# Kernel tuning notes

Hardware: AMD Instinct MI355X
Metric: run time of the kernel (lower is better)

## Reference

```python
import jax, jax.numpy as jnp
import numpy as np

D_MODEL = 256
NUM_HEADS = 4
D_HEAD = D_MODEL // NUM_HEADS
LN_EPS = 1e-5
NEG_INF = -1e9


def setup_inputs() -> dict:
    key = jax.random.key(0)
    ks = jax.random.split(key, 8)
    B, N = 4, 2048
    s = 1.0 / np.sqrt(D_MODEL)
    return {
        "x": jax.random.normal(ks[0], (B, N, D_MODEL), dtype=jnp.float32),
        "Wq": jax.random.normal(ks[1], (D_MODEL, D_MODEL), dtype=jnp.float32) * s,
        "Wk": jax.random.normal(ks[2], (D_MODEL, D_MODEL), dtype=jnp.float32) * s,
        "Wv": jax.random.normal(ks[3], (D_MODEL, D_MODEL), dtype=jnp.float32) * s,
        "Wo": jax.random.normal(ks[4], (D_MODEL, D_MODEL), dtype=jnp.float32) * s,
        "bo": jnp.zeros((D_MODEL,), dtype=jnp.float32),
        "gamma": jnp.ones((D_MODEL,), dtype=jnp.float32),
        "beta": jnp.zeros((D_MODEL,), dtype=jnp.float32),
        "k_neighbors": 8,
    }


def build_knn_adj(x, k):
    # x: [B, N, D]; returns symmetric 0/1 adjacency [B, N, N]
    B, N, _ = x.shape
    xn = x / jnp.maximum(jnp.linalg.norm(x, axis=-1, keepdims=True), 1e-12)
    sim = jnp.einsum('bnd,bmd->bnm', xn, xn)  # [B, N, N]
    _, idx = jax.lax.top_k(sim, k + 1)        # [B, N, k+1]
    b = jnp.arange(B)[:, None, None]
    r = jnp.arange(N)[None, :, None]
    adj = jnp.zeros((B, N, N), dtype=jnp.float32).at[b, r, idx].add(1.0)
    adj = jnp.maximum(adj, jnp.swapaxes(adj, 1, 2))
    return adj


def layer_norm(x, gamma, beta):
    mu = jnp.mean(x, axis=-1, keepdims=True)
    var = jnp.mean(jnp.square(x - mu), axis=-1, keepdims=True)
    return (x - mu) * jax.lax.rsqrt(var + LN_EPS) * gamma + beta


def reference(x, Wq, Wk, Wv, Wo, bo, gamma, beta, k_neighbors):
    B, N, D = x.shape
    adj = build_knn_adj(x, k_neighbors)  # [B, N, N]

    def split_heads(t):  # [B, N, D] -> [B, H, N, d]
        return jnp.transpose(t.reshape(B, N, NUM_HEADS, D_HEAD), (0, 2, 1, 3))

    q = split_heads(x @ Wq)
    k = split_heads(x @ Wk)
    v = split_heads(x @ Wv)

    scores = jnp.einsum('bhnd,bhmd->bhnm', q, k) / jnp.sqrt(jnp.float32(D_HEAD))
    scores = jnp.where(adj[:, None, :, :] > 0, scores, NEG_INF)
    attn = jax.nn.softmax(scores, axis=-1)  # dropout is identity at inference
    out = jnp.einsum('bhnm,bhmd->bhnd', attn, v)
    out = jnp.transpose(out, (0, 2, 1, 3)).reshape(B, N, D)
    out = out @ Wo + bo
    return layer_norm(x + out, gamma, beta)
```

## Files before the change

### kernel.cpp

```cpp
#include <hip/hip_runtime.h>
#include <hip/hip_bf16.h>
#include <math.h>

#define BATCH 4
#define N 2048
#define D 256
#define NH 4
#define DH 64
#define TOPK 9
#define NEG_BIG -1e30f

typedef __bf16 bf16;
typedef __bf16 bf16x4 __attribute__((ext_vector_type(4)));
typedef __bf16 bf16x8 __attribute__((ext_vector_type(8)));
typedef float f32x4 __attribute__((ext_vector_type(4)));

#define PK3(a,b,c) ((a) | ((b) << 2) | ((c) << 4))
#define PK6(a,b,c,d,e,f) ((a) | ((b) << 2) | ((c) << 4) | ((d) << 6) | ((e) << 8) | ((f) << 10))

#define WAITVM(Nc) __builtin_amdgcn_s_waitcnt((((Nc) & 0xf)) | (7u << 4) | (0xfu << 8) | ((((unsigned)(Nc)) >> 4) << 14))

__device__ __forceinline__ void async_cp16(const bf16* g, const bf16* l) {
  __builtin_amdgcn_global_load_lds(
      (const __attribute__((address_space(1))) void*)(uintptr_t)g,
      (__attribute__((address_space(3))) void*)(uintptr_t)l, 16, 0, 0);
}

__global__ __launch_bounds__(64) void prep_kernel(const float* __restrict__ x,
                                                  const float* __restrict__ Wq,
                                                  const float* __restrict__ Wk,
                                                  const float* __restrict__ Wv,
                                                  const float* __restrict__ Wo,
                                                  bf16* __restrict__ XsN,
                                                  bf16* __restrict__ Wt,
                                                  float* __restrict__ norms,
                                                  uint4* __restrict__ mask4) {
  int blk = blockIdx.x;
  int lane = threadIdx.x;
  if (blk < 8192) {
    float4 v = *(const float4*)(x + (size_t)blk * D + lane * 4);
    float ss = v.x * v.x + v.y * v.y + v.z * v.z + v.w * v.w;
    for (int off = 32; off; off >>= 1) ss += __shfl_down(ss, off);
    ss = __shfl(ss, 0);
    float nrm = fmaxf(sqrtf(ss), 1e-12f);
    if (lane == 0) norms[blk] = nrm;
    float sc = 1.0f / nrm;
    float xs[4] = {v.x * sc, v.y * sc, v.z * sc, v.w * sc};
    bf16* o = XsN + (size_t)blk * 512 + lane * 4;
#pragma unroll
    for (int j = 0; j < 4; ++j) {
      float xv = xs[j];
      bf16 h = (bf16)xv;
      o[j] = h;
      o[256 + j] = (bf16)(xv - (float)h);
    }
  } else if (blk < 9216) {
    int jj = blk - 8192;
    const float* W = (jj < 256) ? Wq : (jj < 512) ? Wk : (jj < 768) ? Wv : Wo;
    int j = jj & 255;
    bf16* dst = Wt + (size_t)jj * 512;
    for (int k = lane; k < 256; k += 64) {
      float w = W[(size_t)k * D + j];
      bf16 h = (bf16)w;
      dst[k] = h;
      dst[256 + k] = (bf16)(w - (float)h);
    }
  } else {
    int base = (blk - 9216) * 1024 + lane;
#pragma unroll
    for (int t = 0; t < 16; ++t)
      mask4[base + t * 64] = make_uint4(0, 0, 0, 0);
  }
}

__device__ __forceinline__ void gemm_core(bf16* As, bf16* Bs,
                                          const bf16* __restrict__ Ab,
                                          const bf16* __restrict__ Bb,
                                          void* __restrict__ Cvoid,
                                          int lda, int ldb, int ldc,
                                          int nsteps, int amap, int bmap,
                                          int row0, int col0,
                                          int outmode, bool mirror,
                                          const float* __restrict__ rowscale) {
  int tid = threadIdx.x;
  int lane = tid & 63;
  int wv = tid >> 6;
  int wm = (wv >> 1) * 64;
  int wn = (wv & 1) * 64;

  int rbase = tid >> 2;
  int gperm = (tid & 3) ^ ((rbase >> 1) & 3);
  const bf16* ga0 = Ab + (size_t)rbase * lda + gperm * 8;
  const bf16* gb0 = Bb + (size_t)rbase * ldb + gperm * 8;
  int ldsoff = tid * 8;

  int fr = lane & 15;
  int G = lane >> 4;

  f32x4 acc[4][4] = {};

  auto issue = [&](int st, int buf) {
    int ch = st >> 3;
    int aoff = (((amap >> (ch * 2)) & 3) << 8) | ((st & 7) << 5);
    int boff = (((bmap >> (ch * 2)) & 3) << 8) | ((st & 7) << 5);
#pragma unroll
    for (int q = 0; q < 2; ++q)
      async_cp16(ga0 + (size_t)q * 64 * lda + aoff, &As[buf * 4096 + ldsoff + q * 2048]);
#pragma unroll
    for (int q = 0; q < 2; ++q)
      async_cp16(gb0 + (size_t)q * 64 * ldb + boff, &Bs[buf * 4096 + ldsoff + q * 2048]);
  };

  issue(0, 0);
  for (int st = 0; st < nsteps; ++st) {
    int buf = st & 1;
    if (st + 1 < nsteps) {
      issue(st + 1, buf ^ 1);
      WAITVM(4);
    } else {
      WAITVM(0);
    }
    __builtin_amdgcn_s_barrier();
    bf16x8 af[4], bfr[4];
#pragma unroll
    for (int mi = 0; mi < 4; ++mi) {
      int r = wm + mi * 16 + fr;
      af[mi] = *(const bf16x8*)&As[buf * 4096 + r * 32 + ((G ^ ((r >> 1) & 3)) << 3)];
    }
#pragma unroll
    for (int nj = 0; nj < 4; ++nj) {
      int r = wn + nj * 16 + fr;
      bfr[nj] = *(const bf16x8*)&Bs[buf * 4096 + r * 32 + ((G ^ ((r >> 1) & 3)) << 3)];
    }
#pragma unroll
    for (int mi = 0; mi < 4; ++mi)
#pragma unroll
      for (int nj = 0; nj < 4; ++nj)
        acc[mi][nj] = __builtin_amdgcn_mfma_f32_16x16x32_bf16(af[mi], bfr[nj], acc[mi][nj], 0, 0, 0);
    __builtin_amdgcn_s_barrier();
  }

  int er = (lane >> 4) * 4;
  int ec = lane & 15;
#pragma unroll
  for (int mi = 0; mi < 4; ++mi) {
    int rb = row0 + wm + mi * 16 + er;
    float scl[4] = {1.f, 1.f, 1.f, 1.f};
    if (rowscale) {
      float4 s4 = *(const float4*)(rowscale + rb);
      scl[0] = s4.x; scl[1] = s4.y; scl[2] = s4.z; scl[3] = s4.w;
    }
#pragma unroll
    for (int nj = 0; nj < 4; ++nj) {
      int cb = col0 + wn + nj * 16 + ec;
      if (outmode == 1) {
        float* Cb = (float*)Cvoid;
#pragma unroll
        for (int reg = 0; reg < 4; ++reg)
          __builtin_nontemporal_store(acc[mi][nj][reg],
                                      &Cb[(size_t)(rb + reg) * ldc + cb]);
        if (mirror) {
#pragma unroll
          for (int reg = 0; reg < 4; ++reg)
            __builtin_nontemporal_store(acc[mi][nj][reg],
                                        &Cb[(size_t)cb * ldc + rb + reg]);
        }
      } else {
        bf16* Cb = (bf16*)Cvoid;
#pragma unroll
        for (int reg = 0; reg < 4; ++reg)
          Cb[(size_t)(rb + reg) * ldc + cb] = (bf16)(acc[mi][nj][reg] * scl[reg]);
      }
    }
  }
}

__global__ __launch_bounds__(256, 4) void gemm_sim_kernel(const bf16* __restrict__ XsN,
                                                          float* __restrict__ sim,
                                                          int amap, int bmap) {
  __shared__ bf16 As[2 * 128 * 32];
  __shared__ bf16 Bs[2 * 128 * 32];
  int g = blockIdx.x;
  int xcd = g & 7;
  int slot = g >> 3;
  int z = xcd >> 1;
  int t = (xcd & 1) * 68 + slot;
  int by = 0;
  while (t >= 16 - by) { t -= 16 - by; ++by; }
  int bx = by + t;
  gemm_core(As, Bs,
            XsN + (size_t)z * N * 512 + (size_t)by * 128 * 512,
            XsN + (size_t)z * N * 512 + (size_t)bx * 128 * 512,
            sim + (size_t)z * N * N,
            512, 512, N, 24, amap, bmap, by * 128, bx * 128,
            1, bx != by, nullptr);
}

__global__ __launch_bounds__(256, 4) void gemm_qkv_kernel(const bf16* __restrict__ XsN,
                                                          const bf16* __restrict__ Wt,
                                                          bf16* __restrict__ qkv,
                                                          int amap, int bmap,
                                                          const float* __restrict__ norms) {
  __shared__ bf16 As[2 * 128 * 32];
  __shared__ bf16 Bs[2 * 128 * 32];
  gemm_core(As, Bs,
            XsN + (size_t)blockIdx.y * 128 * 512,
            Wt + (size_t)blockIdx.x * 128 * 512,
            qkv, 512, 512, 768, 16, amap, bmap,
            blockIdx.y * 128, blockIdx.x * 128, 2, false, norms);
}

__global__ __launch_bounds__(256, 4) void gemm_fused_kernel(const bf16* __restrict__ XsN,
                                                            float* __restrict__ sim,
                                                            int amap_s, int bmap_s,
                                                            const bf16* __restrict__ Wt,
                                                            bf16* __restrict__ qkv,
                                                            int amap_q, int bmap_q,
                                                            const float* __restrict__ norms) {
  __shared__ bf16 As[2 * 128 * 32];
  __shared__ bf16 Bs[2 * 128 * 32];
  int g = blockIdx.x;
  if (g < 544) {
    int xcd = g & 7;
    int slot = g >> 3;
    int z = xcd >> 1;
    int t = (xcd & 1) * 68 + slot;
    int by = 0;
    while (t >= 16 - by) { t -= 16 - by; ++by; }
    int bx = by + t;
    gemm_core(As, Bs,
              XsN + (size_t)z * N * 512 + (size_t)by * 128 * 512,
              XsN + (size_t)z * N * 512 + (size_t)bx * 128 * 512,
              sim + (size_t)z * N * N,
              512, 512, N, 24, amap_s, bmap_s, by * 128, bx * 128,
              1, bx != by, nullptr);
  } else {
    int t = g - 544;
    int xcd = t & 7;
    int slot = t >> 3;
    int by = (xcd >> 1) * 16 + (xcd & 1) * 8 + slot / 6;
    int bx = slot % 6;
    gemm_core(As, Bs,
              XsN + (size_t)by * 128 * 512,
              Wt + (size_t)bx * 128 * 512,
              qkv, 512, 512, 768, 16, amap_q, bmap_q,
              by * 128, bx * 128, 2, false, norms);
  }
}

__global__ __launch_bounds__(64) void topk_adj_kernel(const float* __restrict__ sim,
                                                      unsigned* __restrict__ mask) {
  int row = blockIdx.x;
  int lane = threadIdx.x;
  int b = row >> 11, r = row & 2047;
  const float* srow = sim + (size_t)row * N;
  float v[32];
#pragma unroll
  for (int it = 0; it < 8; ++it) {
    float4 q = *(const float4*)(srow + it * 256 + lane * 4);
    v[it * 4 + 0] = q.x; v[it * 4 + 1] = q.y;
    v[it * 4 + 2] = q.z; v[it * 4 + 3] = q.w;
  }
  unsigned removed = 0;
  for (int rs = 0; rs < TOPK; ++rs) {
    float m = -3e38f;
    int mi = 0;
#pragma unroll
    for (int i = 0; i < 32; ++i) {
      float vv = ((removed >> i) & 1u) ? -3e38f : v[i];
      if (vv > m) { m = vv; mi = i; }
    }
    int gidx = ((mi >> 2) << 8) + lane * 4 + (mi & 3);
    for (int off = 32; off; off >>= 1) {
      float om = __shfl_down(m, off);
      int og = __shfl_down(gidx, off);
      if (om > m || (om == m && og < gidx)) { m = om; gidx = og; }
    }
    gidx = __shfl(gidx, 0);
    if (((gidx >> 2) & 63) == lane)
      removed |= 1u << (((gidx >> 8) << 2) | (gidx & 3));
    if (lane == 0) {
      atomicOr(&mask[(size_t)row * 64 + (gidx >> 5)], 1u << (gidx & 31));
      atomicOr(&mask[(((size_t)b << 11) + gidx) * 64 + (r >> 5)], 1u << (r & 31));
    }
  }
}

__global__ __launch_bounds__(256) void attn_kernel(const bf16* __restrict__ qkv,
                                                   const unsigned* __restrict__ mask,
                                                   bf16* __restrict__ aos) {
  __shared__ float sq[4][256];
  __shared__ unsigned short nbr[4][2048];
  __shared__ int s_nn[4];
  int wv = threadIdx.x >> 6;
  int lane = threadIdx.x & 63;
  int g = blockIdx.x;
  int xcd = g & 7;
  int b = xcd >> 1;
  int tile = (xcd & 1) * 256 + (g >> 3);
  int bn = b * N + tile * 4 + wv;
  if (lane == 0) s_nn[wv] = 0;
  {
    bf16x4 qv = *(const bf16x4*)(qkv + (size_t)bn * 768 + lane * 4);
#pragma unroll
    for (int j = 0; j < 4; ++j) sq[wv][lane * 4 + j] = (float)qv[j];
  }
  __syncthreads();
  unsigned bits = mask[(size_t)bn * (N / 32) + lane];
  while (bits) {
    int bit = __ffs(bits) - 1;
    bits &= bits - 1;
    int p = atomicAdd(&s_nn[wv], 1);
    nbr[wv][p] = (unsigned short)(lane * 32 + bit);
  }
  __syncthreads();
  int nn = s_nn[wv];
  const bf16* base = qkv + (size_t)b * N * 768;
  float acc[4] = {0.f, 0.f, 0.f, 0.f};

  auto score4 = [&](int j, float* s) {
    const bf16* kr = base + (size_t)j * 768 + 256;
#pragma unroll
    for (int h = 0; h < 4; ++h) {
      float a = 0.f;
#pragma unroll
      for (int c = 0; c < DH; c += 8) {
        bf16x8 kk = *(const bf16x8*)(kr + h * DH + c);
#pragma unroll
        for (int t = 0; t < 8; ++t) a += sq[wv][h * DH + c + t] * (float)kk[t];
      }
      s[h] = a * 0.125f;
    }
  };

  if (nn <= 64) {
    float s[4] = {NEG_BIG, NEG_BIG, NEG_BIG, NEG_BIG};
    if (lane < nn) score4(nbr[wv][lane], s);
    float w[4], l[4];
#pragma unroll
    for (int h = 0; h < 4; ++h) {
      float m = s[h];
      for (int off = 32; off; off >>= 1) m = fmaxf(m, __shfl_down(m, off));
      m = __shfl(m, 0);
      float e = (lane < nn) ? __expf(s[h] - m) : 0.f;
      float ls = e;
      for (int off = 32; off; off >>= 1) ls += __shfl_down(ls, off);
      l[h] = __shfl(ls, 0);
      w[h] = e;
    }
    int i = 0;
    for (; i + 4 <= nn; i += 4) {
      int j0 = nbr[wv][i + 0], j1 = nbr[wv][i + 1];
      int j2 = nbr[wv][i + 2], j3 = nbr[wv][i + 3];
      const bf16* p0 = base + (size_t)j0 * 768 + 512;
      const bf16* p1 = base + (size_t)j1 * 768 + 512;
      const bf16* p2 = base + (size_t)j2 * 768 + 512;
      const bf16* p3 = base + (size_t)j3 * 768 + 512;
#pragma unroll
      for (int h = 0; h < 4; ++h) {
        acc[h] += __shfl(w[h], i + 0) * (float)p0[h * DH + lane] +
                  __shfl(w[h], i + 1) * (float)p1[h * DH + lane] +
                  __shfl(w[h], i + 2) * (float)p2[h * DH + lane] +
                  __shfl(w[h], i + 3) * (float)p3[h * DH + lane];
      }
    }
    for (; i < nn; ++i) {
      const bf16* p0 = base + (size_t)nbr[wv][i] * 768 + 512;
#pragma unroll
      for (int h = 0; h < 4; ++h) acc[h] += __shfl(w[h], i) * (float)p0[h * DH + lane];
    }
#pragma unroll
    for (int h = 0; h < 4; ++h) acc[h] /= l[h];
  } else {
    float m[4] = {NEG_BIG, NEG_BIG, NEG_BIG, NEG_BIG};
    for (int i0 = 0; i0 < nn; i0 += 64) {
      float s[4] = {NEG_BIG, NEG_BIG, NEG_BIG, NEG_BIG};
      if (i0 + lane < nn) score4(nbr[wv][i0 + lane], s);
#pragma unroll
      for (int h = 0; h < 4; ++h) m[h] = fmaxf(m[h], s[h]);
    }
#pragma unroll
    for (int h = 0; h < 4; ++h) {
      for (int off = 32; off; off >>= 1) m[h] = fmaxf(m[h], __shfl_down(m[h], off));
      m[h] = __shfl(m[h], 0);
    }
    float l[4] = {0.f, 0.f, 0.f, 0.f};
    for (int i0 = 0; i0 < nn; i0 += 64) {
      float s[4] = {NEG_BIG, NEG_BIG, NEG_BIG, NEG_BIG};
      if (i0 + lane < nn) score4(nbr[wv][i0 + lane], s);
      float e[4];
#pragma unroll
      for (int h = 0; h < 4; ++h) {
        e[h] = (i0 + lane < nn) ? __expf(s[h] - m[h]) : 0.f;
        float ls = e[h];
        for (int off = 32; off; off >>= 1) ls += __shfl_down(ls, off);
        l[h] += __shfl(ls, 0);
      }
      int lim = min(64, nn - i0);
      for (int ii = 0; ii < lim; ++ii) {
        const bf16* p0 = base + (size_t)nbr[wv][i0 + ii] * 768 + 512;
#pragma unroll
        for (int h = 0; h < 4; ++h) acc[h] += __shfl(e[h], ii) * (float)p0[h * DH + lane];
      }
    }
#pragma unroll
    for (int h = 0; h < 4; ++h) acc[h] /= l[h];
  }
#pragma unroll
  for (int h = 0; h < 4; ++h) {
    float a = acc[h];
    bf16 hi = (bf16)a;
    aos[(size_t)bn * 512 + h * DH + lane] = hi;
    aos[(size_t)bn * 512 + 256 + h * DH + lane] = (bf16)(a - (float)hi);
  }
}

__global__ __launch_bounds__(256) void projln_kernel(const bf16* __restrict__ A,
                                                     const bf16* __restrict__ Bw,
                                                     const float* __restrict__ x,
                                                     const float* __restrict__ bo,
                                                     const float* __restrict__ gamma,
                                                     const float* __restrict__ beta,
                                                     float* __restrict__ out) {
  __shared__ bf16 As[2 * 32 * 32];
  __shared__ bf16 Bs[2 * 256 * 32];
  __shared__ float rsum[32][4];
  __shared__ float rsq[32][4];
  int tid = threadIdx.x;
  int lane = tid & 63;
  int wv = tid >> 6;
  int wn = wv * 64;
  int row0 = blockIdx.x * 32;

  int rt = tid >> 2;
  int ra = tid >> 2;
  int gpa = (tid & 3) ^ ((ra >> 1) & 3);
  const bf16* ga0 = A + (size_t)(row0 + ra) * 512 + gpa * 8;

  int fr = lane & 15;
  int G = lane >> 4;

  f32x4 acc[2][4] = {};

  auto issue = [&](int st, int buf) {
    int aoff = ((st >> 3) << 8) | ((st & 7) << 5);
    int boff = (st & 7) << 5;
    if (tid < 128)
      async_cp16(ga0 + aoff, &As[buf * 1024 + tid * 8]);
#pragma unroll
    for (int q = 0; q < 4; ++q) {
      int rb = q * 64 + rt;
      int gpb = (tid & 3) ^ ((rb >> 1) & 3);
      async_cp16(Bw + (size_t)rb * 512 + gpb * 8 + boff,
                 &Bs[buf * 8192 + (q * 256 + tid) * 8]);
    }
  };

  issue(0, 0);
  for (int st = 0; st < 16; ++st) {
    int buf = st & 1;
    if (st + 1 < 16) {
      issue(st + 1, buf ^ 1);
      WAITVM(4);
    } else {
      WAITVM(0);
    }
    __builtin_amdgcn_s_barrier();
    bf16x8 af[2], bfr[4];
#pragma unroll
    for (int mi = 0; mi < 2; ++mi) {
      int r = mi * 16 + fr;
      af[mi] = *(const bf16x8*)&As[buf * 1024 + r * 32 + ((G ^ ((r >> 1) & 3)) << 3)];
    }
#pragma unroll
    for (int nj = 0; nj < 4; ++nj) {
      int r = wn + nj * 16 + fr;
      bfr[nj] = *(const bf16x8*)&Bs[buf * 8192 + r * 32 + ((G ^ ((r >> 1) & 3)) << 3)];
    }
#pragma unroll
    for (int mi = 0; mi < 2; ++mi)
#pragma unroll
      for (int nj = 0; nj < 4; ++nj)
        acc[mi][nj] = __builtin_amdgcn_mfma_f32_16x16x32_bf16(af[mi], bfr[nj], acc[mi][nj], 0, 0, 0);
    __builtin_amdgcn_s_barrier();
  }

  int er = (lane >> 4) * 4;
  int ec = lane & 15;
  float bo_c[4], ga_c[4], be_c[4];
#pragma unroll
  for (int nj = 0; nj < 4; ++nj) {
    int c = wn + nj * 16 + ec;
    bo_c[nj] = bo[c]; ga_c[nj] = gamma[c]; be_c[nj] = beta[c];
  }
#pragma unroll
  for (int mi = 0; mi < 2; ++mi)
#pragma unroll
    for (int reg = 0; reg < 4; ++reg) {
      int rloc = mi * 16 + er + reg;
      const float* xr = x + (size_t)(row0 + rloc) * D;
      float su = 0.f, s2 = 0.f;
#pragma unroll
      for (int nj = 0; nj < 4; ++nj) {
        float u = acc[mi][nj][reg] + bo_c[nj] + xr[wn + nj * 16 + ec];
        su += u; s2 += u * u;
      }
#pragma unroll
      for (int m = 1; m <= 8; m <<= 1) {
        su += __shfl_xor(su, m);
        s2 += __shfl_xor(s2, m);
      }
      if (ec == 0) { rsum[rloc][wv] = su; rsq[rloc][wv] = s2; }
    }
  __syncthreads();
#pragma unroll
  for (int mi = 0; mi < 2; ++mi)
#pragma unroll
    for (int reg = 0; reg < 4; ++reg) {
      int rloc = mi * 16 + er + reg;
      float s = rsum[rloc][0] + rsum[rloc][1] + rsum[rloc][2] + rsum[rloc][3];
      float q2 = rsq[rloc][0] + rsq[rloc][1] + rsq[rloc][2] + rsq[rloc][3];
      float mean = s * (1.0f / D);
      float var = q2 * (1.0f / D) - mean * mean;
      float rstd = rsqrtf(var + 1e-5f);
      const float* xr = x + (size_t)(row0 + rloc) * D;
      float* orow = out + (size_t)(row0 + rloc) * D;
#pragma unroll
      for (int nj = 0; nj < 4; ++nj) {
        float u = acc[mi][nj][reg] + bo_c[nj] + xr[wn + nj * 16 + ec];
        orow[wn + nj * 16 + ec] = (u - mean) * rstd * ga_c[nj] + be_c[nj];
      }
    }
}

extern "C" void kernel_launch(void* const* d_in, const int* in_sizes, int n_in,
                              void* d_out, int out_size, void* d_ws, size_t ws_size,
                              hipStream_t stream) {
  const float* x     = (const float*)d_in[0];
  const float* Wq    = (const float*)d_in[1];
  const float* Wk    = (const float*)d_in[2];
  const float* Wv    = (const float*)d_in[3];
  const float* Wo    = (const float*)d_in[4];
  const float* bo    = (const float*)d_in[5];
  const float* gamma = (const float*)d_in[6];
  const float* beta  = (const float*)d_in[7];
  float* out = (float*)d_out;

  char* ws = (char*)d_ws;
  bf16* XsN      = (bf16*)(ws);
  float* sim     = (float*)(ws + 12582912);
  float* norms   = (float*)(ws + 79691776);
  unsigned* mask = (unsigned*)(ws + 79986688);
  bf16* Wt       = (bf16*)(ws + 82083840);

  bool big = ws_size >= (size_t)125000000;
  bf16* qkv = (bf16*)(ws + (big ? 83132416 : 12582912));
  bf16* aos = (bf16*)(ws + (big ? 95715328 : 37748736));

  const int AMAP_SIM = PK6(0, 0, 1, 0, 0, 0);
  const int BMAP_SIM = PK6(0, 1, 0, 0, 0, 0);
  const int AMAP_2T  = PK3(0, 1, 0);
  const int BMAP_2T  = PK3(0, 0, 1);

  prep_kernel<<<9344, 64, 0, stream>>>(x, Wq, Wk, Wv, Wo, XsN, Wt, norms,
                                       (uint4*)mask);

  if (big) {
    gemm_fused_kernel<<<928, 256, 0, stream>>>(
        XsN, sim, AMAP_SIM, BMAP_SIM, Wt, qkv, AMAP_2T, BMAP_2T, norms);
    topk_adj_kernel<<<BATCH * N, 64, 0, stream>>>(sim, mask);
  } else {
    gemm_sim_kernel<<<544, 256, 0, stream>>>(XsN, sim, AMAP_SIM, BMAP_SIM);
    topk_adj_kernel<<<BATCH * N, 64, 0, stream>>>(sim, mask);
    gemm_qkv_kernel<<<dim3(6, 64), 256, 0, stream>>>(XsN, Wt, qkv,
                                                     AMAP_2T, BMAP_2T, norms);
  }

  attn_kernel<<<(BATCH * N) / 4, 256, 0, stream>>>(qkv, mask, aos);

  projln_kernel<<<256, 256, 0, stream>>>(aos, Wt + (size_t)768 * 512,
                                         x, bo, gamma, beta, out);
}
```

Baseline: 186.4 us.

## Replace 128x128 fused GEMM with 256x256-tile, 8-wave MFMA kernel

Replaces the fused similarity/QKV GEMM, which used 128x128 tiles with 4 waves, by a 256x256-tile kernel with 8 waves. It uses a 64-wide K slab in 128KB of LDS, split-phase staging of A and B with async global-to-LDS copies, and s_setprio around the MFMA bursts. Grid scheduling is remapped to 144 symmetric sim tiles plus 96 QKV tiles, with XCD-aware placement. The goal is higher arithmetic intensity and less global/LDS traffic per FLOP. The cost is fewer blocks (240), so occupancy and load balance across CUs drop.

New measurement: 189.8 us. Within noise of the previous version (+1.9%).

```diff
diff --git a/kernel.cpp b/kernel.cpp
--- a/kernel.cpp
+++ b/kernel.cpp
@@ -73,6 +73,190 @@
   }
 }
 
+__device__ __forceinline__ void gemm_core256(bf16* S,
+                                             const bf16* __restrict__ Ab,
+                                             const bf16* __restrict__ Bb,
+                                             void* __restrict__ Cvoid,
+                                             int ldc, int ntiles,
+                                             int amap, int bmap,
+                                             int row0, int col0,
+                                             int outmode, bool mirror,
+                                             const float* __restrict__ rowscale) {
+  int tid = threadIdx.x;
+  int lane = tid & 63;
+  int wv = tid >> 6;
+  int wm = (wv >> 2) * 128;
+  int wn = (wv & 3) * 64;
+  int aht = wv >> 2;
+  int bht = 2 + ((wv & 3) >> 1);
+  int brow = (wv & 1) * 64;
+
+  int fr = lane & 15;
+  int fq = lane >> 4;
+
+  int s0 = tid, s1 = tid + 512;
+  int r0 = s0 >> 3, sl0 = s0 & 7;
+  int r1 = s1 >> 3, sl1 = s1 & 7;
+  int gc0 = (sl0 ^ (r0 & 7)) << 3;
+  int gc1 = (sl1 ^ (r1 & 7)) << 3;
+
+  f32x4 acc[8][4] = {};
+
+  auto koffs = [&](int kt, int map) {
+    return (((map >> ((kt >> 2) * 2)) & 3) << 8) | ((kt & 3) << 6);
+  };
+  auto stageAB = [&](int kt, int buf, int half01) {
+    const bf16* Base = half01 ? Bb : Ab;
+    int koff = koffs(kt, half01 ? bmap : amap);
+    bf16* d = S + buf * 32768 + half01 * 16384;
+    const bf16* b0 = Base + koff;
+    async_cp16(b0 + (size_t)r0 * 512 + gc0, d + s0 * 8);
+    async_cp16(b0 + (size_t)r1 * 512 + gc1, d + s1 * 8);
+    async_cp16(b0 + (size_t)(128 + r0) * 512 + gc0, d + 8192 + s0 * 8);
+    async_cp16(b0 + (size_t)(128 + r1) * 512 + gc1, d + 8192 + s1 * 8);
+  };
+  auto readA = [&](bf16x8* af, int buf, int hm, int ks) {
+#pragma unroll
+    for (int i = 0; i < 4; ++i) {
+      int r = hm * 64 + i * 16 + fr;
+      int c = ks * 4 + fq;
+      af[i] = *(const bf16x8*)&S[buf * 32768 + aht * 8192 + r * 64 + ((c ^ (r & 7)) << 3)];
+    }
+  };
+  auto readB = [&](bf16x8* bb, int buf, int ks) {
+#pragma unroll
+    for (int nj = 0; nj < 4; ++nj) {
+      int r = brow + nj * 16 + fr;
+      int c = ks * 4 + fq;
+      bb[nj] = *(const bf16x8*)&S[buf * 32768 + bht * 8192 + r * 64 + ((c ^ (r & 7)) << 3)];
+    }
+  };
+
+  stageAB(0, 0, 0);
+  stageAB(0, 0, 1);
+  WAITVM(0);
+  __builtin_amdgcn_s_barrier();
+
+  for (int kt = 0; kt < ntiles; ++kt) {
+    int buf = kt & 1;
+    bool more = (kt + 1 < ntiles);
+    bf16x8 af[4], bb[4];
+    readB(bb, buf, 0);
+    readA(af, buf, 0, 0);
+    if (more) stageAB(kt + 1, buf ^ 1, 0);
+    __builtin_amdgcn_s_barrier();
+    __builtin_amdgcn_s_setprio(1);
+#pragma unroll
+    for (int i = 0; i < 4; ++i)
+#pragma unroll
+      for (int nj = 0; nj < 4; ++nj)
+        acc[i][nj] = __builtin_amdgcn_mfma_f32_16x16x32_bf16(af[i], bb[nj], acc[i][nj], 0, 0, 0);
+    __builtin_amdgcn_s_setprio(0);
+    __builtin_amdgcn_s_barrier();
+    readA(af, buf, 1, 0);
+    if (more) stageAB(kt + 1, buf ^ 1, 1);
+    __builtin_amdgcn_s_barrier();
+    __builtin_amdgcn_s_setprio(1);
+#pragma unroll
+    for (int i = 0; i < 4; ++i)
+#pragma unroll
+      for (int nj = 0; nj < 4; ++nj)
+        acc[4 + i][nj] = __builtin_amdgcn_mfma_f32_16x16x32_bf16(af[i], bb[nj], acc[4 + i][nj], 0, 0, 0);
+    __builtin_amdgcn_s_setprio(0);
+    __builtin_amdgcn_s_barrier();
+    readB(bb, buf, 1);
+    readA(af, buf, 0, 1);
+    __builtin_amdgcn_s_barrier();
+    __builtin_amdgcn_s_setprio(1);
+#pragma unroll
+    for (int i = 0; i < 4; ++i)
+#pragma unroll
+      for (int nj = 0; nj < 4; ++nj)
+        acc[i][nj] = __builtin_amdgcn_mfma_f32_16x16x32_bf16(af[i], bb[nj], acc[i][nj], 0, 0, 0);
+    __builtin_amdgcn_s_setprio(0);
+    __builtin_amdgcn_s_barrier();
+    readA(af, buf, 1, 1);
+    __builtin_amdgcn_s_barrier();
+    __builtin_amdgcn_s_setprio(1);
+#pragma unroll
+    for (int i = 0; i < 4; ++i)
+#pragma unroll
+      for (int nj = 0; nj < 4; ++nj)
+        acc[4 + i][nj] = __builtin_amdgcn_mfma_f32_16x16x32_bf16(af[i], bb[nj], acc[4 + i][nj], 0, 0, 0);
+    __builtin_amdgcn_s_setprio(0);
+    WAITVM(0);
+    __builtin_amdgcn_s_barrier();
+  }
+
+  int er = (lane >> 4) * 4;
+  int ec = lane & 15;
+#pragma unroll
+  for (int mi = 0; mi < 8; ++mi) {
+    int rb = row0 + wm + mi * 16 + er;
+    float scl[4] = {1.f, 1.f, 1.f, 1.f};
+    if (rowscale) {
+      float4 s4 = *(const float4*)(rowscale + rb);
+      scl[0] = s4.x; scl[1] = s4.y; scl[2] = s4.z; scl[3] = s4.w;
+    }
+#pragma unroll
+    for (int nj = 0; nj < 4; ++nj) {
+      int cb = col0 + wn + nj * 16 + ec;
+      if (outmode == 1) {
+        float* Cb = (float*)Cvoid;
+#pragma unroll
+        for (int reg = 0; reg < 4; ++reg)
+          __builtin_nontemporal_store(acc[mi][nj][reg],
+                                      &Cb[(size_t)(rb + reg) * ldc + cb]);
+        if (mirror) {
+#pragma unroll
+          for (int reg = 0; reg < 4; ++reg)
+            __builtin_nontemporal_store(acc[mi][nj][reg],
+                                        &Cb[(size_t)cb * ldc + rb + reg]);
+        }
+      } else {
+        bf16* Cb = (bf16*)Cvoid;
+#pragma unroll
+        for (int reg = 0; reg < 4; ++reg)
+          Cb[(size_t)(rb + reg) * ldc + cb] = (bf16)(acc[mi][nj][reg] * scl[reg]);
+      }
+    }
+  }
+}
+
+__global__ __launch_bounds__(512, 2) void gemm_fused256_kernel(
+    const bf16* __restrict__ XsN, float* __restrict__ sim,
+    int amap_s, int bmap_s,
+    const bf16* __restrict__ Wt, bf16* __restrict__ qkv,
+    int amap_q, int bmap_q, const float* __restrict__ norms) {
+  __shared__ bf16 S[65536];
+  int g = blockIdx.x;
+  if (g < 144) {
+    int xcd = g & 7;
+    int z = xcd >> 1;
+    int t = (xcd & 1) * 18 + (g >> 3);
+    int by = 0;
+    while (t >= 8 - by) { t -= 8 - by; ++by; }
+    int bx = by + t;
+    gemm_core256(S,
+                 XsN + (size_t)z * N * 512 + (size_t)by * 256 * 512,
+                 XsN + (size_t)z * N * 512 + (size_t)bx * 256 * 512,
+                 sim + (size_t)z * N * N,
+                 N, 12, amap_s, bmap_s, by * 256, bx * 256,
+                 1, bx != by, nullptr);
+  } else {
+    int t = g - 144;
+    int xcd = t & 7;
+    int slot = t >> 3;
+    int by = (xcd >> 1) * 8 + (xcd & 1) * 4 + slot / 3;
+    int bx = slot % 3;
+    gemm_core256(S,
+                 XsN + (size_t)by * 256 * 512,
+                 Wt + (size_t)bx * 256 * 512,
+                 qkv, 768, 8, amap_q, bmap_q,
+                 by * 256, bx * 256, 2, false, norms);
+  }
+}
+
 __device__ __forceinline__ void gemm_core(bf16* As, bf16* Bs,
                                           const bf16* __restrict__ Ab,
                                           const bf16* __restrict__ Bb,
@@ -210,44 +394,6 @@
             blockIdx.y * 128, blockIdx.x * 128, 2, false, norms);
 }
 
-__global__ __launch_bounds__(256, 4) void gemm_fused_kernel(const bf16* __restrict__ XsN,
-                                                            float* __restrict__ sim,
-                                                            int amap_s, int bmap_s,
-                                                            const bf16* __restrict__ Wt,
-                                                            bf16* __restrict__ qkv,
-                                                            int amap_q, int bmap_q,
-                                                            const float* __restrict__ norms) {
-  __shared__ bf16 As[2 * 128 * 32];
-  __shared__ bf16 Bs[2 * 128 * 32];
-  int g = blockIdx.x;
-  if (g < 544) {
-    int xcd = g & 7;
-    int slot = g >> 3;
-    int z = xcd >> 1;
-    int t = (xcd & 1) * 68 + slot;
-    int by = 0;
-    while (t >= 16 - by) { t -= 16 - by; ++by; }
-    int bx = by + t;
-    gemm_core(As, Bs,
-              XsN + (size_t)z * N * 512 + (size_t)by * 128 * 512,
-              XsN + (size_t)z * N * 512 + (size_t)bx * 128 * 512,
-              sim + (size_t)z * N * N,
-              512, 512, N, 24, amap_s, bmap_s, by * 128, bx * 128,
-              1, bx != by, nullptr);
-  } else {
-    int t = g - 544;
-    int xcd = t & 7;
-    int slot = t >> 3;
-    int by = (xcd >> 1) * 16 + (xcd & 1) * 8 + slot / 6;
-    int bx = slot % 6;
-    gemm_core(As, Bs,
-              XsN + (size_t)by * 128 * 512,
-              Wt + (size_t)bx * 128 * 512,
-              qkv, 512, 512, 768, 16, amap_q, bmap_q,
-              by * 128, bx * 128, 2, false, norms);
-  }
-}
-
 __global__ __launch_bounds__(64) void topk_adj_kernel(const float* __restrict__ sim,
                                                       unsigned* __restrict__ mask) {
   int row = blockIdx.x;
@@ -566,7 +712,7 @@
                                        (uint4*)mask);
 
   if (big) {
-    gemm_fused_kernel<<<928, 256, 0, stream>>>(
+    gemm_fused256_kernel<<<240, 512, 0, stream>>>(
         XsN, sim, AMAP_SIM, BMAP_SIM, Wt, qkv, AMAP_2T, BMAP_2T, norms);
     topk_adj_kernel<<<BATCH * N, 64, 0, stream>>>(sim, mask);
   } else {
```

## Use 128x256 block tiles for fused similarity and QKV GEMM

Applied to the files above, without the earlier changes.

Replaces the 128x128-tile fused GEMM kernel with a 128x256-tile variant. Each wave now computes a 64x128 sub-tile, which doubles B-operand reuse per loaded A fragment and halves the block count from 928 to 480, with the triangular sim tile scheduling remapped to match. The cost is more accumulator registers and a lower occupancy target (2 blocks per CU), plus fewer blocks to balance across the GPU.

Result: no change. 187.8 us (+0.7%).

```diff
diff --git a/kernel.cpp b/kernel.cpp
--- a/kernel.cpp
+++ b/kernel.cpp
@@ -73,6 +73,149 @@
   }
 }
 
+__device__ __forceinline__ void gemm_core128x256(bf16* As, bf16* Bs,
+                                                 const bf16* __restrict__ Ab,
+                                                 const bf16* __restrict__ Bb,
+                                                 void* __restrict__ Cvoid,
+                                                 int ldc, int nsteps,
+                                                 int amap, int bmap,
+                                                 int row0, int col0,
+                                                 int outmode, bool mirror,
+                                                 const float* __restrict__ rowscale) {
+  int tid = threadIdx.x;
+  int lane = tid & 63;
+  int wv = tid >> 6;
+  int wm = (wv >> 1) * 64;
+  int wn = (wv & 1) * 128;
+  int fr = lane & 15;
+  int G = lane >> 4;
+
+  f32x4 acc[4][8] = {};
+
+  auto issue = [&](int st, int buf) {
+    int ch = st >> 3;
+    int aoff = (((amap >> (ch * 2)) & 3) << 8) | ((st & 7) << 5);
+    int boff = (((bmap >> (ch * 2)) & 3) << 8) | ((st & 7) << 5);
+#pragma unroll
+    for (int q = 0; q < 2; ++q) {
+      int s = q * 256 + tid;
+      int r = s >> 2, sl = s & 3;
+      async_cp16(Ab + (size_t)r * 512 + ((sl ^ ((r >> 1) & 3)) << 3) + aoff,
+                 &As[buf * 4096 + s * 8]);
+    }
+#pragma unroll
+    for (int q = 0; q < 4; ++q) {
+      int s = q * 256 + tid;
+      int r = s >> 2, sl = s & 3;
+      async_cp16(Bb + (size_t)r * 512 + ((sl ^ ((r >> 1) & 3)) << 3) + boff,
+                 &Bs[buf * 8192 + s * 8]);
+    }
+  };
+
+  issue(0, 0);
+  for (int st = 0; st < nsteps; ++st) {
+    int buf = st & 1;
+    if (st + 1 < nsteps) {
+      issue(st + 1, buf ^ 1);
+      WAITVM(6);
+    } else {
+      WAITVM(0);
+    }
+    __builtin_amdgcn_s_barrier();
+    bf16x8 af[4], bfr[8];
+#pragma unroll
+    for (int mi = 0; mi < 4; ++mi) {
+      int r = wm + mi * 16 + fr;
+      af[mi] = *(const bf16x8*)&As[buf * 4096 + r * 32 + ((G ^ ((r >> 1) & 3)) << 3)];
+    }
+#pragma unroll
+    for (int nj = 0; nj < 8; ++nj) {
+      int r = wn + nj * 16 + fr;
+      bfr[nj] = *(const bf16x8*)&Bs[buf * 8192 + r * 32 + ((G ^ ((r >> 1) & 3)) << 3)];
+    }
+    __builtin_amdgcn_s_setprio(1);
+#pragma unroll
+    for (int mi = 0; mi < 4; ++mi)
+#pragma unroll
+      for (int nj = 0; nj < 8; ++nj)
+        acc[mi][nj] = __builtin_amdgcn_mfma_f32_16x16x32_bf16(af[mi], bfr[nj], acc[mi][nj], 0, 0, 0);
+    __builtin_amdgcn_s_setprio(0);
+    __builtin_amdgcn_s_barrier();
+  }
+
+  int er = (lane >> 4) * 4;
+  int ec = lane & 15;
+#pragma unroll
+  for (int mi = 0; mi < 4; ++mi) {
+    int rb = row0 + wm + mi * 16 + er;
+    float scl[4] = {1.f, 1.f, 1.f, 1.f};
+    if (rowscale) {
+      float4 s4 = *(const float4*)(rowscale + rb);
+      scl[0] = s4.x; scl[1] = s4.y; scl[2] = s4.z; scl[3] = s4.w;
+    }
+#pragma unroll
+    for (int nj = 0; nj < 8; ++nj) {
+      int cb = col0 + wn + nj * 16 + ec;
+      if (outmode == 1) {
+        float* Cb = (float*)Cvoid;
+#pragma unroll
+        for (int reg = 0; reg < 4; ++reg)
+          __builtin_nontemporal_store(acc[mi][nj][reg],
+                                      &Cb[(size_t)(rb + reg) * ldc + cb]);
+        if (mirror) {
+          __builtin_nontemporal_store(acc[mi][nj],
+                                      (f32x4*)&Cb[(size_t)cb * ldc + rb]);
+        }
+      } else {
+        bf16* Cb = (bf16*)Cvoid;
+#pragma unroll
+        for (int reg = 0; reg < 4; ++reg)
+          Cb[(size_t)(rb + reg) * ldc + cb] = (bf16)(acc[mi][nj][reg] * scl[reg]);
+      }
+    }
+  }
+}
+
+__global__ __launch_bounds__(256, 2) void gemm_fused128x256_kernel(
+    const bf16* __restrict__ XsN, float* __restrict__ sim,
+    int amap_s, int bmap_s,
+    const bf16* __restrict__ Wt, bf16* __restrict__ qkv,
+    int amap_q, int bmap_q, const float* __restrict__ norms) {
+  __shared__ bf16 As[2 * 128 * 32];
+  __shared__ bf16 Bs[2 * 256 * 32];
+  int g = blockIdx.x;
+  if (g < 288) {
+    int xcd = g & 7;
+    int z = xcd >> 1;
+    int t = (xcd & 1) * 36 + (g >> 3);
+    int half = t & 1;
+    int u = t >> 1;
+    int by = 0;
+    while (u >= 8 - by) { u -= 8 - by; ++by; }
+    int bx = by + u;
+    int row0 = by * 256 + half * 128;
+    int col0 = bx * 256;
+    gemm_core128x256(As, Bs,
+                     XsN + (size_t)z * N * 512 + (size_t)row0 * 512,
+                     XsN + (size_t)z * N * 512 + (size_t)col0 * 512,
+                     sim + (size_t)z * N * N,
+                     N, 24, amap_s, bmap_s, row0, col0,
+                     1, bx != by, nullptr);
+  } else {
+    int t = g - 288;
+    int xcd = t & 7;
+    int slot = t >> 3;
+    int z = xcd >> 1;
+    int by = z * 16 + (xcd & 1) * 8 + slot / 3;
+    int bx = slot % 3;
+    gemm_core128x256(As, Bs,
+                     XsN + (size_t)by * 128 * 512,
+                     Wt + (size_t)bx * 256 * 512,
+                     qkv, 768, 16, amap_q, bmap_q,
+                     by * 128, bx * 256, 2, false, norms);
+  }
+}
+
 __device__ __forceinline__ void gemm_core(bf16* As, bf16* Bs,
                                           const bf16* __restrict__ Ab,
                                           const bf16* __restrict__ Bb,
@@ -210,44 +353,6 @@
             blockIdx.y * 128, blockIdx.x * 128, 2, false, norms);
 }
 
-__global__ __launch_bounds__(256, 4) void gemm_fused_kernel(const bf16* __restrict__ XsN,
-                                                            float* __restrict__ sim,
-                                                            int amap_s, int bmap_s,
-                                                            const bf16* __restrict__ Wt,
-                                                            bf16* __restrict__ qkv,
-                                                            int amap_q, int bmap_q,
-                                                            const float* __restrict__ norms) {
-  __shared__ bf16 As[2 * 128 * 32];
-  __shared__ bf16 Bs[2 * 128 * 32];
-  int g = blockIdx.x;
-  if (g < 544) {
-    int xcd = g & 7;
-    int slot = g >> 3;
-    int z = xcd >> 1;
-    int t = (xcd & 1) * 68 + slot;
-    int by = 0;
-    while (t >= 16 - by) { t -= 16 - by; ++by; }
-    int bx = by + t;
-    gemm_core(As, Bs,
-              XsN + (size_t)z * N * 512 + (size_t)by * 128 * 512,
-              XsN + (size_t)z * N * 512 + (size_t)bx * 128 * 512,
-              sim + (size_t)z * N * N,
-              512, 512, N, 24, amap_s, bmap_s, by * 128, bx * 128,
-              1, bx != by, nullptr);
-  } else {
-    int t = g - 544;
-    int xcd = t & 7;
-    int slot = t >> 3;
-    int by = (xcd >> 1) * 16 + (xcd & 1) * 8 + slot / 6;
-    int bx = slot % 6;
-    gemm_core(As, Bs,
-              XsN + (size_t)by * 128 * 512,
-              Wt + (size_t)bx * 128 * 512,
-              qkv, 512, 512, 768, 16, amap_q, bmap_q,
-              by * 128, bx * 128, 2, false, norms);
-  }
-}
-
 __global__ __launch_bounds__(64) void topk_adj_kernel(const float* __restrict__ sim,
                                                       unsigned* __restrict__ mask) {
   int row = blockIdx.x;
@@ -566,7 +671,7 @@
                                        (uint4*)mask);
 
   if (big) {
-    gemm_fused_kernel<<<928, 256, 0, stream>>>(
+    gemm_fused128x256_kernel<<<480, 256, 0, stream>>>(
         XsN, sim, AMAP_SIM, BMAP_SIM, Wt, qkv, AMAP_2T, BMAP_2T, norms);
     topk_adj_kernel<<<BATCH * N, 64, 0, stream>>>(sim, mask);
   } else {
```
